# Performance work log

Measured on AMD Instinct MI355X. Metric: run time of the kernel, lower is better.

The kernel has to match this reference:

```python
import jax, jax.numpy as jnp
import numpy as np

B, D, L = 8, 512, 2000          # batch, encoder_out_dim, seq_len
E = 300                          # embedding_dim
N1, N2 = 118, 8929               # hierarchy level sizes


def setup_inputs() -> dict:
    key = jax.random.key(0)
    k = jax.random.split(key, 6)
    H = jax.random.normal(k[0], (B, D, L), dtype=jnp.float32)
    Q1w = jax.random.normal(k[1], (N1, E), dtype=jnp.float32) * 0.05   # cat_embedding_matrix
    Q2w = jax.random.normal(k[2], (N2, E), dtype=jnp.float32) * 0.05   # label_embedding_matrix
    # Q12: xavier_uniform over [N2, N1]
    bound = float(np.sqrt(6.0 / (N1 + N2)))
    Q12w = jax.random.uniform(k[3], (N2, N1), minval=-bound, maxval=bound, dtype=jnp.float32)
    # 1x1 conv mapping: weight [D, E], bias [D] (kernel_size=1 squeezed)
    cbound = float(np.sqrt(1.0 / E))
    Wmap = jax.random.uniform(k[4], (D, E), minval=-cbound, maxval=cbound, dtype=jnp.float32)
    bmap = jax.random.uniform(k[5], (D,), minval=-cbound, maxval=cbound, dtype=jnp.float32)
    return {"H": H, "Q1w": Q1w, "Q2w": Q2w, "Q12w": Q12w, "Wmap": Wmap, "bmap": bmap}


def reference(H, Q1w, Q2w, Q12w, Wmap, bmap):
    # 1x1 conv mapping == affine map over embedding dim: [n, E] @ [E, D] + b
    Q1 = Q1w @ Wmap.T + bmap                      # [N1, D]
    E1 = jnp.einsum('nd,bdl->bnl', Q1, H)         # level-1 scores [B, N1, L]
    A1 = jax.nn.softmax(E1, axis=2)
    C1 = jnp.einsum('bnl,bdl->bnd', A1, H)        # [B, N1, D]
    C1 = jnp.einsum('mn,bnd->bmd', Q12w, C1)      # project to level 2: [B, N2, D]
    Q2 = (Q2w @ Wmap.T + bmap) * C1               # [N2, D] * [B, N2, D]
    E2 = jnp.einsum('bmd,bdl->bml', Q2, H)        # level-2 scores [B, N2, L]
    A2 = jax.nn.softmax(E2, axis=2)
    C2 = jnp.einsum('bml,bdl->bmd', A2, H)        # [B, N2, D]
    return (C2, A2)
```

## Files before the change

### kernel.cpp

```cpp
#include <hip/hip_runtime.h>

typedef short    bf16x8 __attribute__((ext_vector_type(8)));
typedef float    f32x4  __attribute__((ext_vector_type(4)));
typedef unsigned short u16x8 __attribute__((ext_vector_type(8)));

__device__ __forceinline__ unsigned short f2bf(float f) {
    unsigned u = __float_as_uint(f);
    return (unsigned short)((u + 0x7fffu + ((u >> 16) & 1u)) >> 16);
}
__device__ __forceinline__ float bf2f(unsigned short h) {
    return __uint_as_float((unsigned)h << 16);
}

template<bool> struct otype            { using T = float; };
template<>     struct otype<true>      { using T = unsigned short; };

template<int BM,int BN,int TM,int TN,bool BT,bool VA,bool VB,bool OB>
__launch_bounds__(256)
__global__ void gemm_f32(const float* __restrict__ A, int lda, long long sA,
                         const float* __restrict__ B, int ldb, long long sB,
                         void* __restrict__ Cv, int ldc, long long sC,
                         int M, int N, int K,
                         const float* __restrict__ bias,
                         const float* __restrict__ mul, int mulld)
{
    constexpr int BK  = 16;
    constexpr int GSA = BM*4/TM;
    constexpr int GSB = BN*4/TN;
    __shared__ float As[BK][BM+4];
    __shared__ float Bs[BK][BN+4];

    const int bz = blockIdx.z;
    A += (long long)bz * sA;
    B += (long long)bz * sB;
    using OT = typename otype<OB>::T;
    OT* C = (OT*)Cv + (long long)bz * sC;
    const int m0 = blockIdx.y * BM;
    const int n0 = blockIdx.x * BN;
    const int tid = threadIdx.x;
    const int tm = tid >> 4;
    const int tn = tid & 15;

    float acc[TM][TN];
#pragma unroll
    for (int i=0;i<TM;++i)
#pragma unroll
        for (int j=0;j<TN;++j) acc[i][j]=0.f;

    for (int k0=0;k0<K;k0+=BK) {
        if constexpr (VA) {
#pragma unroll
            for (int r=0;r<BM*BK/1024;++r) {
                int v = tid + r*256;
                int m = v >> 2, k4 = (v & 3)*4;
                int gm = m0+m, gk = k0+k4;
                float4 val = make_float4(0.f,0.f,0.f,0.f);
                if (gm < M) {
                    if (gk+3 < K) {
                        val = *reinterpret_cast<const float4*>(A + (long long)gm*lda + gk);
                    } else {
                        float t0 = (gk   < K) ? A[(long long)gm*lda+gk  ] : 0.f;
                        float t1 = (gk+1 < K) ? A[(long long)gm*lda+gk+1] : 0.f;
                        float t2 = (gk+2 < K) ? A[(long long)gm*lda+gk+2] : 0.f;
                        val = make_float4(t0,t1,t2,0.f);
                    }
                }
                As[k4+0][m]=val.x; As[k4+1][m]=val.y; As[k4+2][m]=val.z; As[k4+3][m]=val.w;
            }
        } else {
#pragma unroll
            for (int r=0;r<BM*BK/256;++r) {
                int e = tid + r*256;
                int m = e >> 4, k = e & 15;
                int gm=m0+m, gk=k0+k;
                As[k][m] = (gm<M && gk<K) ? A[(long long)gm*lda+gk] : 0.f;
            }
        }
        if constexpr (!BT) {
            if constexpr (VB) {
#pragma unroll
                for (int r=0;r<BK*BN/1024;++r) {
                    int v = tid + r*256;
                    int k = v / (BN/4), n4 = (v % (BN/4))*4;
                    int gk=k0+k, gn=n0+n4;
                    float4 val = make_float4(0.f,0.f,0.f,0.f);
                    if (gk < K) {
                        if (gn+3 < N) {
                            val = *reinterpret_cast<const float4*>(B + (long long)gk*ldb + gn);
                        } else {
                            float t0=(gn  <N)?B[(long long)gk*ldb+gn  ]:0.f;
                            float t1=(gn+1<N)?B[(long long)gk*ldb+gn+1]:0.f;
                            float t2=(gn+2<N)?B[(long long)gk*ldb+gn+2]:0.f;
                            val = make_float4(t0,t1,t2,0.f);
                        }
                    }
                    Bs[k][n4+0]=val.x; Bs[k][n4+1]=val.y; Bs[k][n4+2]=val.z; Bs[k][n4+3]=val.w;
                }
            } else {
#pragma unroll
                for (int r=0;r<BK*BN/256;++r) {
                    int e = tid + r*256;
                    int k = e / BN, n = e % BN;
                    int gk=k0+k, gn=n0+n;
                    Bs[k][n] = (gk<K && gn<N) ? B[(long long)gk*ldb+gn] : 0.f;
                }
            }
        } else {
            if constexpr (VB) {
#pragma unroll
                for (int r=0;r<BN*BK/1024;++r) {
                    int v = tid + r*256;
                    int n = v >> 2, k4 = (v&3)*4;
                    int gn=n0+n, gk=k0+k4;
                    float4 val = make_float4(0.f,0.f,0.f,0.f);
                    if (gn < N) {
                        if (gk+3 < K) {
                            val = *reinterpret_cast<const float4*>(B + (long long)gn*ldb + gk);
                        } else {
                            float t0=(gk  <K)?B[(long long)gn*ldb+gk  ]:0.f;
                            float t1=(gk+1<K)?B[(long long)gn*ldb+gk+1]:0.f;
                            float t2=(gk+2<K)?B[(long long)gn*ldb+gk+2]:0.f;
                            val=make_float4(t0,t1,t2,0.f);
                        }
                    }
                    Bs[k4+0][n]=val.x; Bs[k4+1][n]=val.y; Bs[k4+2][n]=val.z; Bs[k4+3][n]=val.w;
                }
            } else {
#pragma unroll
                for (int r=0;r<BN*BK/256;++r) {
                    int e = tid + r*256;
                    int n = e >> 4, k = e & 15;
                    int gn=n0+n, gk=k0+k;
                    Bs[k][n] = (gn<N && gk<K) ? B[(long long)gn*ldb+gk] : 0.f;
                }
            }
        }
        __syncthreads();
#pragma unroll
        for (int kk=0;kk<BK;++kk) {
            float a[TM], bb[TN];
#pragma unroll
            for (int g=0;g<TM/4;++g) {
                float4 t = *reinterpret_cast<const float4*>(&As[kk][g*GSA + tm*4]);
                a[4*g+0]=t.x; a[4*g+1]=t.y; a[4*g+2]=t.z; a[4*g+3]=t.w;
            }
#pragma unroll
            for (int g=0;g<TN/4;++g) {
                float4 t = *reinterpret_cast<const float4*>(&Bs[kk][g*GSB + tn*4]);
                bb[4*g+0]=t.x; bb[4*g+1]=t.y; bb[4*g+2]=t.z; bb[4*g+3]=t.w;
            }
#pragma unroll
            for (int i=0;i<TM;++i)
#pragma unroll
                for (int j=0;j<TN;++j)
                    acc[i][j] = fmaf(a[i], bb[j], acc[i][j]);
        }
        __syncthreads();
    }
#pragma unroll
    for (int i=0;i<TM;++i) {
        int row = m0 + (i>>2)*GSA + tm*4 + (i&3);
        if (row < M) {
#pragma unroll
            for (int j=0;j<TN;++j) {
                int col = n0 + (j>>2)*GSB + tn*4 + (j&3);
                if (col < N) {
                    float val = acc[i][j];
                    if (bias) val += bias[col];
                    if (mul)  val *= mul[(long long)row*mulld + col];
                    if constexpr (OB) C[(long long)row*ldc + col] = f2bf(val);
                    else              C[(long long)row*ldc + col] = val;
                }
            }
        }
    }
}

template<unsigned F>
__launch_bounds__(512, 4)
__global__ void gemm_mfma_p(const unsigned short* __restrict__ A, int lda, long long sA,
                            const unsigned short* __restrict__ Bt, int ldb, long long sB,
                            void* __restrict__ Cv, int ldc, long long sC,
                            int M, int Ncols, int NX, int NY, int NT,
                            const float* __restrict__ bias,
                            const float* __restrict__ mul, int ldm,
                            float* __restrict__ partial, long long pstride,
                            const float* __restrict__ hsum,
                            const float* __restrict__ invs,
                            float* __restrict__ a2out,
                            float* __restrict__ dump)
{
    __shared__ unsigned short lds[3][12288];

    const int nwg = gridDim.x;
    const int q = nwg >> 3, r = nwg & 7;
    const int xcd = blockIdx.x & 7, idx = blockIdx.x >> 3;
    const int wg = (xcd < r ? xcd*(q+1) : r*(q+1) + (xcd-r)*q) + idx;
    const int nx = wg % NX;
    const int t1 = wg / NX;
    const int my = t1 % NY;
    const int bz = t1 / NY;

    const int tid  = threadIdx.x;
    const int lane = tid & 63, wid = tid >> 6;
    const int wr = wid >> 2, wc = wid & 3;
    const int fr = lane & 15, fq = lane >> 4;
    const int m0 = my * 128;
    const int n0 = nx * 256;

    A  += (long long)bz * sA;
    Bt += (long long)bz * sB;

    const int srow = tid >> 2;
    const int scz  = (tid & 3) ^ ((srow >> 1) & 3);
    long long arow = m0 + srow; if (arow > M-1) arow = M-1;
    const unsigned short* aSrc  = A  + arow*lda + scz*8;
    const unsigned short* bSrc0 = Bt + (long long)(n0 + srow)*ldb + scz*8;
    const unsigned short* bSrc1 = bSrc0 + 128ll*ldb;

    bool a2ok = false;
    int  par  = 0;
    float invv = 0.f;
    float* a2p = nullptr;
    if constexpr ((F & 64) != 0) {
        par = nx & 1;
        const int rrow = m0 + srow;
        a2ok = rrow < M;
        const long long ridx = (long long)bz*M + (a2ok ? rrow : M-1);
        invv = invs[ridx];
        asm volatile("" : "+v"(invv));
        a2p = a2out + ridx*2000ll;
    }

    int aoff[4], boff[4];
#pragma unroll
    for (int m=0;m<4;++m) {
        const int ra = wr*64 + m*16 + fr;
        aoff[m] = ra*64 + ((fq ^ ((ra>>1)&3))*16);
    }
#pragma unroll
    for (int n=0;n<4;++n) {
        const int rb = wc*64 + n*16 + fr;
        boff[n] = 8192 + rb*64 + ((fq ^ ((rb>>1)&3))*16);
    }

    f32x4 acc[4][4];
#pragma unroll
    for (int i=0;i<4;++i)
#pragma unroll
        for (int j=0;j<4;++j) acc[i][j] = (f32x4)(0.f);

    auto stage = [&](int s, int t) {
        const int koff = t*32;
        char* base = (char*)&lds[s][0];
        __builtin_amdgcn_global_load_lds(
            (const __attribute__((address_space(1))) void*)(aSrc + koff),
            (__attribute__((address_space(3))) void*)(base + tid*16), 16, 0, 0);
        __builtin_amdgcn_global_load_lds(
            (const __attribute__((address_space(1))) void*)(bSrc0 + koff),
            (__attribute__((address_space(3))) void*)(base + 8192 + tid*16), 16, 0, 0);
        __builtin_amdgcn_global_load_lds(
            (const __attribute__((address_space(1))) void*)(bSrc1 + koff),
            (__attribute__((address_space(3))) void*)(base + 16384 + tid*16), 16, 0, 0);
    };

    stage(0, 0);
    stage(1, NT > 1 ? 1 : 0);
    asm volatile("s_waitcnt vmcnt(3)" ::: "memory");
    __builtin_amdgcn_s_barrier();

    int cur = 0, stg = 2;
    for (int kt = 0; kt < NT; ++kt) {
        int tnx = kt + 2; if (tnx > NT-1) tnx = NT-1;
        stage(stg, tnx);
        const char* bp = (const char*)&lds[cur][0];
        bf16x8 a[4], b[4];
#pragma unroll
        for (int m=0;m<4;++m) a[m] = *(const bf16x8*)(bp + aoff[m]);
#pragma unroll
        for (int n=0;n<4;++n) b[n] = *(const bf16x8*)(bp + boff[n]);
        __builtin_amdgcn_s_setprio(1);
#pragma unroll
        for (int m=0;m<4;++m)
#pragma unroll
            for (int n=0;n<4;++n)
                acc[m][n] = __builtin_amdgcn_mfma_f32_16x16x32_bf16(a[m], b[n], acc[m][n], 0, 0, 0);
        __builtin_amdgcn_s_setprio(0);
        if constexpr ((F & 64) != 0) {
            if ((kt & 1) == par) {
                u16x8 av = *(const u16x8*)(bp + (tid << 4));
                const int col0 = kt*32 + scz*8;
                const bool ok = a2ok && (col0 < 2000);
                float* p0 = ok ? (a2p + col0) : (dump + (tid << 3));
                float4 o0, o1;
                o0.x = fmaf(bf2f((unsigned short)av[0]), invv, invv);
                o0.y = fmaf(bf2f((unsigned short)av[1]), invv, invv);
                o0.z = fmaf(bf2f((unsigned short)av[2]), invv, invv);
                o0.w = fmaf(bf2f((unsigned short)av[3]), invv, invv);
                o1.x = fmaf(bf2f((unsigned short)av[4]), invv, invv);
                o1.y = fmaf(bf2f((unsigned short)av[5]), invv, invv);
                o1.z = fmaf(bf2f((unsigned short)av[6]), invv, invv);
                o1.w = fmaf(bf2f((unsigned short)av[7]), invv, invv);
                *(float4*)(p0    ) = o0;
                *(float4*)(p0 + 4) = o1;
            }
        }
        asm volatile("s_waitcnt lgkmcnt(0)" ::: "memory");
        if constexpr ((F & 64) != 0) {
            asm volatile("s_waitcnt vmcnt(5)" ::: "memory");
        } else {
            asm volatile("s_waitcnt vmcnt(3)" ::: "memory");
        }
        __builtin_amdgcn_s_barrier();
        cur = (cur == 2) ? 0 : cur + 1;
        stg = (stg == 2) ? 0 : stg + 1;
    }

    if constexpr ((F & 16) != 0) {
        __shared__ float sp[4][128];
        unsigned short* Cb = (unsigned short*)Cv + (long long)bz * sC;
        float rp[4][4];
#pragma unroll
        for (int m=0;m<4;++m)
#pragma unroll
            for (int j=0;j<4;++j) rp[m][j] = 0.f;
#pragma unroll
        for (int m=0;m<4;++m) {
            const int rb = m0 + wr*64 + m*16 + fq*4;
#pragma unroll
            for (int n=0;n<4;++n) {
                const int col = n0 + wc*64 + n*16 + fr;
#pragma unroll
                for (int j=0;j<4;++j) {
                    float x = __expf(acc[m][n][j]) - 1.0f;
                    rp[m][j] += x;
                    const int row = rb + j;
                    if (row < M) Cb[(long long)row*ldc + col] = f2bf(x);
                }
            }
        }
#pragma unroll
        for (int m=0;m<4;++m)
#pragma unroll
            for (int j=0;j<4;++j) {
                float s = rp[m][j];
                s += __shfl_xor(s, 1); s += __shfl_xor(s, 2);
                s += __shfl_xor(s, 4); s += __shfl_xor(s, 8);
                rp[m][j] = s;
            }
        if (fr == 0) {
#pragma unroll
            for (int m=0;m<4;++m)
#pragma unroll
                for (int j=0;j<4;++j)
                    sp[wc][wr*64 + m*16 + fq*4 + j] = rp[m][j];
        }
        __syncthreads();
        if (tid < 128) {
            const int row = m0 + tid;
            if (row < M) {
                float s = sp[0][tid] + sp[1][tid] + sp[2][tid] + sp[3][tid];
                partial[(long long)nx*pstride + (long long)bz*M + row] = s;
            }
        }
    } else if constexpr ((F & 8) != 0) {
        unsigned short* Ct = (unsigned short*)Cv + (long long)bz * sC;
#pragma unroll
        for (int m=0;m<4;++m) {
            const int rb = m0 + wr*64 + m*16 + fq*4;
#pragma unroll
            for (int n=0;n<4;++n) {
                const int col = n0 + wc*64 + n*16 + fr;
                if (col < Ncols) {
                    float hv = 0.f;
                    if constexpr ((F & 32) != 0) hv = hsum[(long long)bz*Ncols + col];
#pragma unroll
                    for (int j=0;j<4;++j) {
                        const int row = rb + j;
                        float val = 0.f;
                        if (row < M) {
                            val = acc[m][n][j];
                            if constexpr ((F & 32) != 0) val = (val + hv) * invs[(long long)bz*M + row];
                        }
                        Ct[(long long)col*ldc + row] = f2bf(val);
                    }
                }
            }
        }
    } else {
        float*          Cf = (float*)Cv + (long long)bz * sC;
        unsigned short* Cb = (unsigned short*)Cv + (long long)bz * sC;
#pragma unroll
        for (int m=0;m<4;++m) {
            const int rb = m0 + wr*64 + m*16 + fq*4;
#pragma unroll
            for (int n=0;n<4;++n) {
                const int col = n0 + wc*64 + n*16 + fr;
                if (col < Ncols) {
                    float bv = 0.f, hv = 0.f;
                    if constexpr ((F & 1) != 0) bv = bias[col];
                    if constexpr ((F & 32) != 0) hv = hsum[(long long)bz*Ncols + col];
#pragma unroll
                    for (int j=0;j<4;++j) {
                        const int row = rb + j;
                        if (row < M) {
                            float val = acc[m][n][j];
                            if constexpr ((F & 1)   != 0) val += bv;
                            if constexpr ((F & 2)   != 0) val *= mul[(long long)row*ldm + col];
                            if constexpr ((F & 128) != 0) val *= bf2f(((const unsigned short*)mul)[(long long)row*ldm + col]);
                            if constexpr ((F & 32)  != 0) val = (val + hv) * invs[(long long)bz*M + row];
                            if constexpr ((F & 4)   != 0) Cb[(long long)row*ldc + col] = f2bf(val);
                            else                          Cf[(long long)row*ldc + col] = val;
                        }
                    }
                }
            }
        }
    }
}

template<bool AF32>
__launch_bounds__(512, 2)
__global__ void gemm_mfma(const void* __restrict__ Ain, int lda, long long sA,
                          const unsigned short* __restrict__ Bt, int ldb, long long sB,
                          float* __restrict__ C, int ldc, long long sC,
                          int M, int N, int K, int NT)
{
    __shared__ unsigned short As[2][128*32];
    __shared__ unsigned short Bs[2][256*32];

    const int tid  = threadIdx.x;
    const int lane = tid & 63, wid = tid >> 6;
    const int wr = wid >> 2, wc = wid & 3;
    const int fr = lane & 15, fq = lane >> 4;
    const int bz = blockIdx.z;
    const int m0 = blockIdx.y * 128;
    const int n0 = blockIdx.x * 256;

    const unsigned short* Ab = nullptr;
    const float*          Af = nullptr;
    if constexpr (AF32) Af = (const float*)Ain + (long long)bz * sA;
    else                Ab = (const unsigned short*)Ain + (long long)bz * sA;
    Bt += (long long)bz * sB;
    C  += (long long)bz * sC;

    const int srow = tid >> 2;
    const int sc   = tid & 3;
    const int scz  = sc ^ ((srow >> 1) & 3);
    int arow = m0 + srow; if (arow > M-1) arow = M-1;
    const bool am_ok = (m0 + srow) < M;
    const long long brow0 = n0 + srow;
    const long long brow1 = n0 + 128 + srow;
    const int ldsA  = wid << 10;
    const int ldsB0 = wid << 10;
    const int ldsB1 = 8192 + (wid << 10);

    f32x4 acc[4][4];
#pragma unroll
    for (int i=0;i<4;++i)
#pragma unroll
        for (int j=0;j<4;++j) acc[i][j] = (f32x4)(0.f);

    auto stage = [&](int buf, int t) {
        const long long koff = (long long)t * 32;
        __builtin_amdgcn_global_load_lds(
            (const __attribute__((address_space(1))) void*)(Bt + brow0*ldb + koff + scz*8),
            (__attribute__((address_space(3))) void*)((char*)&Bs[buf][0] + ldsB0), 16, 0, 0);
        __builtin_amdgcn_global_load_lds(
            (const __attribute__((address_space(1))) void*)(Bt + brow1*ldb + koff + scz*8),
            (__attribute__((address_space(3))) void*)((char*)&Bs[buf][0] + ldsB1), 16, 0, 0);
        if constexpr (!AF32) {
            __builtin_amdgcn_global_load_lds(
                (const __attribute__((address_space(1))) void*)(Ab + (long long)arow*lda + koff + scz*8),
                (__attribute__((address_space(3))) void*)((char*)&As[buf][0] + ldsA), 16, 0, 0);
        } else {
            const float* src = Af + (long long)arow*lda + koff + scz*8;
            const int kk = t*32 + scz*8;
            float4 z = make_float4(0.f,0.f,0.f,0.f);
            float4 v0 = (am_ok && kk   < K) ? *(const float4*)(src  ) : z;
            float4 v1 = (am_ok && kk+4 < K) ? *(const float4*)(src+4) : z;
            u16x8 o;
            o[0]=f2bf(v0.x); o[1]=f2bf(v0.y); o[2]=f2bf(v0.z); o[3]=f2bf(v0.w);
            o[4]=f2bf(v1.x); o[5]=f2bf(v1.y); o[6]=f2bf(v1.z); o[7]=f2bf(v1.w);
            *(u16x8*)((char*)&As[buf][0] + tid*16) = o;
        }
    };

    stage(0, 0);
    int cur = 0;
    for (int t = 0; t < NT; ++t) {
        __syncthreads();
        if (t + 1 < NT) stage(cur ^ 1, t + 1);
        const unsigned short* as = As[cur];
        const unsigned short* bs = Bs[cur];
        bf16x8 a[4], b[4];
#pragma unroll
        for (int m=0;m<4;++m) {
            const int ra = wr*64 + m*16 + fr;
            a[m] = *(const bf16x8*)(as + ra*32 + (fq ^ ((ra>>1)&3))*8);
        }
#pragma unroll
        for (int n=0;n<4;++n) {
            const int rb = wc*64 + n*16 + fr;
            b[n] = *(const bf16x8*)(bs + rb*32 + (fq ^ ((rb>>1)&3))*8);
        }
        __builtin_amdgcn_s_setprio(1);
#pragma unroll
        for (int m=0;m<4;++m)
#pragma unroll
            for (int n=0;n<4;++n)
                acc[m][n] = __builtin_amdgcn_mfma_f32_16x16x32_bf16(a[m], b[n], acc[m][n], 0, 0, 0);
        __builtin_amdgcn_s_setprio(0);
        cur ^= 1;
    }
#pragma unroll
    for (int m=0;m<4;++m) {
        const int rb = m0 + wr*64 + m*16 + fq*4;
#pragma unroll
        for (int n=0;n<4;++n) {
            const int col = n0 + wc*64 + n*16 + fr;
            if (col < N) {
#pragma unroll
                for (int j=0;j<4;++j) {
                    const int row = rb + j;
                    if (row < M) C[(long long)row*ldc + col] = acc[m][n][j];
                }
            }
        }
    }
}

__global__ __launch_bounds__(256) void mega_prep(const float* __restrict__ H,
                                                 unsigned short* __restrict__ Hb,
                                                 unsigned short* __restrict__ Htb,
                                                 float* __restrict__ hpart,
                                                 const float* __restrict__ Wmap,  unsigned short* __restrict__ Wb,
                                                 const float* __restrict__ Q1w,   unsigned short* __restrict__ Q1wb,
                                                 const float* __restrict__ Q2w,   unsigned short* __restrict__ Q2wb,
                                                 const float* __restrict__ Q12w,  unsigned short* __restrict__ Q12wb)
{
    __shared__ unsigned short T[64][80];
    const int tid = threadIdx.x;
    int id = blockIdx.x;
    if (id < 2048) {
        const int lt = id & 31;
        const int dt = (id >> 5) & 7;
        const int bz = id >> 8;
        const int d0 = dt * 64;
        const int l0 = lt * 64;
        const float* Hsrc = H + ((long long)bz*512 + d0) * 2000;
        const int dl = tid >> 2;
        const int lc = (tid & 3) * 16;
        float4 v[4];
        float s = 0.f;
#pragma unroll
        for (int i=0;i<4;++i) {
            const int gl = l0 + lc + i*4;
            v[i] = make_float4(0.f,0.f,0.f,0.f);
            if (gl < 2000) v[i] = *(const float4*)(Hsrc + (long long)dl*2000 + gl);
            s += (v[i].x + v[i].y) + (v[i].z + v[i].w);
            T[lc+i*4+0][dl] = f2bf(v[i].x);
            T[lc+i*4+1][dl] = f2bf(v[i].y);
            T[lc+i*4+2][dl] = f2bf(v[i].z);
            T[lc+i*4+3][dl] = f2bf(v[i].w);
        }
        {
            unsigned short* hb = Hb + ((long long)bz*512 + d0 + dl)*2048 + l0 + lc;
            u16x8 h0, h1;
            h0[0]=f2bf(v[0].x); h0[1]=f2bf(v[0].y); h0[2]=f2bf(v[0].z); h0[3]=f2bf(v[0].w);
            h0[4]=f2bf(v[1].x); h0[5]=f2bf(v[1].y); h0[6]=f2bf(v[1].z); h0[7]=f2bf(v[1].w);
            h1[0]=f2bf(v[2].x); h1[1]=f2bf(v[2].y); h1[2]=f2bf(v[2].z); h1[3]=f2bf(v[2].w);
            h1[4]=f2bf(v[3].x); h1[5]=f2bf(v[3].y); h1[6]=f2bf(v[3].z); h1[7]=f2bf(v[3].w);
            *(u16x8*)(hb    ) = h0;
            *(u16x8*)(hb + 8) = h1;
        }
        s += __shfl_xor(s, 1);
        s += __shfl_xor(s, 2);
        if ((tid & 3) == 0)
            hpart[(long long)lt*4096 + bz*512 + d0 + dl] = s;
        __syncthreads();
        unsigned short* Hdst = Htb + ((long long)bz*2048 + l0) * 512 + d0;
        const int ll = tid >> 2;
        const int dc = (tid & 3) * 16;
        u16x8 w0 = *(const u16x8*)&T[ll][dc];
        u16x8 w1 = *(const u16x8*)&T[ll][dc+8];
        *(u16x8*)(Hdst + (long long)ll*512 + dc    ) = w0;
        *(u16x8*)(Hdst + (long long)ll*512 + dc + 8) = w1;
        return;
    }
    id -= 2048;
    const float* src; unsigned short* dst; long long tot; int sc, dc;
    if (id < 640)        { src=Wmap;  dst=Wb;    tot=512ll*320;  sc=300; dc=320; }
    else if (id < 788)   { id-=640;   src=Q1w;   dst=Q1wb;  tot=118ll*320;  sc=300; dc=320; }
    else if (id < 11950) { id-=788;   src=Q2w;   dst=Q2wb;  tot=8929ll*320; sc=300; dc=320; }
    else                 { id-=11950; src=Q12w;  dst=Q12wb; tot=8929ll*128; sc=118; dc=128; }
    const long long i = (long long)id*256 + tid;
    if (i < tot) {
        const long long rr = i / dc;
        const int c = (int)(i - rr*dc);
        dst[i] = (c < sc) ? f2bf(src[rr*sc + c]) : (unsigned short)0;
    }
}

__global__ __launch_bounds__(256) void reduce_hsum(const float* __restrict__ hpart,
                                                   float* __restrict__ Hsum)
{
    const int r = blockIdx.x*256 + threadIdx.x;
    float s = 0.f;
#pragma unroll
    for (int i=0;i<32;++i) s += hpart[(long long)i*4096 + r];
    Hsum[r] = s;
}

__global__ __launch_bounds__(256) void invs_k(const float* __restrict__ partial,
                                              long long pstride,
                                              float* __restrict__ invs, int n)
{
    const int r = blockIdx.x*256 + threadIdx.x;
    if (r < n) {
        float s = 0.f;
#pragma unroll
        for (int i=0;i<8;++i) s += partial[i*pstride + r];
        invs[r] = 1.0f / (2000.0f + s);
    }
}

__global__ __launch_bounds__(256) void cvt_pad_bf16(const float* __restrict__ H,
                                                    unsigned short* __restrict__ Hb)
{
    const long long idx = (long long)blockIdx.x * 256 + threadIdx.x;
    const long long row = idx >> 8;
    const int l0 = (int)(idx & 255) * 8;
    u16x8 o = (u16x8)(unsigned short)0;
    if (l0 + 8 <= 2000) {
        const float* s = H + row*2000 + l0;
        float4 v0 = *(const float4*)(s);
        float4 v1 = *(const float4*)(s+4);
        o[0]=f2bf(v0.x); o[1]=f2bf(v0.y); o[2]=f2bf(v0.z); o[3]=f2bf(v0.w);
        o[4]=f2bf(v1.x); o[5]=f2bf(v1.y); o[6]=f2bf(v1.z); o[7]=f2bf(v1.w);
    }
    *(u16x8*)(Hb + row*2048 + l0) = o;
}

__global__ __launch_bounds__(256) void cvt_transpose_bf16(const float* __restrict__ H,
                                                          unsigned short* __restrict__ Ht)
{
    __shared__ unsigned short T[64][80];
    const int bz = blockIdx.z;
    const int d0 = blockIdx.y * 64;
    const int l0 = blockIdx.x * 64;
    const float* Hsrc = H + ((long long)bz*512 + d0) * 2000;
    unsigned short* Hdst = Ht + ((long long)bz*2048 + l0) * 512 + d0;
    const int tid = threadIdx.x;
    const int dl = tid >> 2;
    const int lc = (tid & 3) * 16;
#pragma unroll
    for (int i=0;i<4;++i) {
        const int l = lc + i*4;
        const int gl = l0 + l;
        float4 v = make_float4(0.f,0.f,0.f,0.f);
        if (gl < 2000) v = *(const float4*)(Hsrc + (long long)dl*2000 + gl);
        T[l+0][dl] = f2bf(v.x);
        T[l+1][dl] = f2bf(v.y);
        T[l+2][dl] = f2bf(v.z);
        T[l+3][dl] = f2bf(v.w);
    }
    __syncthreads();
    const int ll = tid >> 2;
    const int dc = (tid & 3) * 16;
    u16x8 w0 = *(const u16x8*)&T[ll][dc];
    u16x8 w1 = *(const u16x8*)&T[ll][dc+8];
    *(u16x8*)(Hdst + (long long)ll*512 + dc    ) = w0;
    *(u16x8*)(Hdst + (long long)ll*512 + dc + 8) = w1;
}

__global__ __launch_bounds__(256) void softmax_rows(float* __restrict__ X, int L,
                                                    unsigned short* __restrict__ Xb, int Lb)
{
    const long long row = blockIdx.x;
    float* x = X + row * (long long)L;
    const int tid = threadIdx.x;
    const int nv = L >> 2;
    const bool h0 = tid < nv;
    const bool h1 = tid + 256 < nv;
    float4 t0 = make_float4(0.f,0.f,0.f,0.f);
    float4 t1 = make_float4(0.f,0.f,0.f,0.f);
    float mx = -3.402823e38f;
    if (h0) { t0 = *reinterpret_cast<const float4*>(x + 4*tid);
              mx = fmaxf(fmaxf(t0.x,t0.y), fmaxf(t0.z,t0.w)); }
    if (h1) { t1 = *reinterpret_cast<const float4*>(x + 4*(tid+256));
              mx = fmaxf(mx, fmaxf(fmaxf(t1.x,t1.y), fmaxf(t1.z,t1.w))); }
    __shared__ float sred[4];
#pragma unroll
    for (int o=32;o;o>>=1) mx = fmaxf(mx, __shfl_xor(mx, o));
    if ((tid & 63)==0) sred[tid>>6] = mx;
    __syncthreads();
    mx = fmaxf(fmaxf(sred[0],sred[1]), fmaxf(sred[2],sred[3]));
    __syncthreads();
    float s = 0.f;
    if (h0) {
        t0.x=__expf(t0.x-mx); t0.y=__expf(t0.y-mx); t0.z=__expf(t0.z-mx); t0.w=__expf(t0.w-mx);
        s += (t0.x+t0.y)+(t0.z+t0.w);
    }
    if (h1) {
        t1.x=__expf(t1.x-mx); t1.y=__expf(t1.y-mx); t1.z=__expf(t1.z-mx); t1.w=__expf(t1.w-mx);
        s += (t1.x+t1.y)+(t1.z+t1.w);
    }
#pragma unroll
    for (int o=32;o;o>>=1) s += __shfl_xor(s, o);
    if ((tid & 63)==0) sred[tid>>6] = s;
    __syncthreads();
    s = (sred[0]+sred[1])+(sred[2]+sred[3]);
    const float inv = 1.0f / s;
    if (h0) { t0.x*=inv; t0.y*=inv; t0.z*=inv; t0.w*=inv;
              *reinterpret_cast<float4*>(x + 4*tid) = t0; }
    if (h1) { t1.x*=inv; t1.y*=inv; t1.z*=inv; t1.w*=inv;
              *reinterpret_cast<float4*>(x + 4*(tid+256)) = t1; }
    if (Xb) {
        unsigned short* xb = Xb + row * (long long)Lb;
        if (h0) {
            ushort4 o; o.x=f2bf(t0.x); o.y=f2bf(t0.y); o.z=f2bf(t0.z); o.w=f2bf(t0.w);
            *reinterpret_cast<ushort4*>(xb + 4*tid) = o;
        }
        if (h1) {
            ushort4 o; o.x=f2bf(t1.x); o.y=f2bf(t1.y); o.z=f2bf(t1.z); o.w=f2bf(t1.w);
            *reinterpret_cast<ushort4*>(xb + 4*(tid+256)) = o;
        }
        if (tid < (Lb - L)/4) {
            ushort4 z; z.x=z.y=z.z=z.w=0;
            *reinterpret_cast<ushort4*>(xb + L + 4*tid) = z;
        }
    }
}

extern "C" void kernel_launch(void* const* d_in, const int* in_sizes, int n_in,
                              void* d_out, int out_size, void* d_ws, size_t ws_size,
                              hipStream_t stream)
{
    const float* H    = (const float*)d_in[0];
    const float* Q1w  = (const float*)d_in[1];
    const float* Q2w  = (const float*)d_in[2];
    const float* Q12w = (const float*)d_in[3];
    const float* Wmap = (const float*)d_in[4];
    const float* bmap = (const float*)d_in[5];

    constexpr long long B=8, D=512, L=2000, N1=118, N2=8929;
    constexpr long long C2E = B*N2*D;
    float* out = (float*)d_out;
    float* C2  = out;
    float* A2  = out + C2E;

    dim3 blk(256);

    size_t off = 0;
    auto alloc = [&](size_t n)->size_t { off = (off + 255) & ~(size_t)255; size_t o = off; off += n; return o; };
    const size_t oHb    = alloc(8ll*512*2048*2);
    const size_t oHtb   = alloc(8ll*2048*512*2);
    const size_t oWb    = alloc(512ll*320*2);
    const size_t oQ1wb  = alloc(118ll*320*2);
    const size_t oQ2wb  = alloc(8929ll*320*2);
    const size_t oQ12wb = alloc(8929ll*128*2);
    const size_t oQ1b   = alloc(118ll*512*2);
    const size_t oEmbb  = alloc(8929ll*512*2);
    const size_t oE1x   = alloc(8ll*128*2048*2);
    const size_t oC1tb  = alloc(8ll*512*128*2);
    const size_t oQ2b   = alloc(8ll*8929*512*2);
    const size_t oA2b   = alloc(8ll*8929*2048*2);
    const size_t oPart  = alloc(8ll*8*8929*4);
    const size_t oPart1 = alloc(8ll*944*4);
    const size_t oInvs  = alloc(8ll*8929*4);
    const size_t oInvs1 = alloc(944ll*4);
    const size_t oHsum  = alloc(8ll*512*4);
    const size_t oHpart = alloc(32ll*4096*4);
    const size_t FULL_NEED = off;

    char* ws = (char*)d_ws;

    if (ws_size >= FULL_NEED) {
        unsigned short* Hb    = (unsigned short*)(ws + oHb);
        unsigned short* Htb   = (unsigned short*)(ws + oHtb);
        unsigned short* Wb    = (unsigned short*)(ws + oWb);
        unsigned short* Q1wb  = (unsigned short*)(ws + oQ1wb);
        unsigned short* Q2wb  = (unsigned short*)(ws + oQ2wb);
        unsigned short* Q12wb = (unsigned short*)(ws + oQ12wb);
        unsigned short* Q1b   = (unsigned short*)(ws + oQ1b);
        unsigned short* Embb  = (unsigned short*)(ws + oEmbb);
        unsigned short* E1x   = (unsigned short*)(ws + oE1x);
        unsigned short* C1tb  = (unsigned short*)(ws + oC1tb);
        unsigned short* Q2b   = (unsigned short*)(ws + oQ2b);
        unsigned short* A2b   = (unsigned short*)(ws + oA2b);
        float*          part  = (float*)(ws + oPart);
        float*          part1 = (float*)(ws + oPart1);
        float*          invs  = (float*)(ws + oInvs);
        float*          invs1 = (float*)(ws + oInvs1);
        float*          Hsum  = (float*)(ws + oHsum);
        float*          hpart = (float*)(ws + oHpart);

        mega_prep<<<dim3(18464), blk, 0, stream>>>(H, Hb, Htb, hpart,
                                                   Wmap, Wb, Q1w, Q1wb, Q2w, Q2wb, Q12w, Q12wb);
        reduce_hsum<<<dim3(16), blk, 0, stream>>>(hpart, Hsum);

        gemm_mfma_p<5><<<dim3(2), dim3(512), 0, stream>>>(
            Q1wb, 320, 0, Wb, 320, 0, Q1b, 512, 0, 118, 512, 2, 1, 10,
            bmap, nullptr, 0, nullptr, 0, nullptr, nullptr, nullptr, nullptr);
        gemm_mfma_p<5><<<dim3(140), dim3(512), 0, stream>>>(
            Q2wb, 320, 0, Wb, 320, 0, Embb, 512, 0, 8929, 512, 2, 70, 10,
            bmap, nullptr, 0, nullptr, 0, nullptr, nullptr, nullptr, nullptr);
        gemm_mfma_p<16><<<dim3(64), dim3(512), 0, stream>>>(
            Q1b, 512, 0, Htb, 512, 2048*512, E1x, 2048, 128*2048, 118, 2048, 8, 1, 16,
            nullptr, nullptr, 0, part1, 944, nullptr, nullptr, nullptr, nullptr);
        invs_k<<<dim3(4), blk, 0, stream>>>(part1, 944, invs1, 944);
        gemm_mfma_p<40><<<dim3(16), dim3(512), 0, stream>>>(
            E1x, 2048, 128*2048, Hb, 2048, 512*2048, C1tb, 128, 512*128, 118, 512, 2, 1, 64,
            nullptr, nullptr, 0, nullptr, 0, Hsum, invs1, nullptr, nullptr);
        gemm_mfma_p<132><<<dim3(1120), dim3(512), 0, stream>>>(
            Q12wb, 128, 0, C1tb, 128, 512*128, Q2b, 512, N2*D, 8929, 512, 2, 70, 4,
            nullptr, (const float*)Embb, 512, nullptr, 0, nullptr, nullptr, nullptr, nullptr);
        gemm_mfma_p<16><<<dim3(4480), dim3(512), 0, stream>>>(
            Q2b, 512, N2*D, Htb, 512, 2048*512, A2b, 2048, N2*2048, 8929, 2048, 8, 70, 16,
            nullptr, nullptr, 0, part, 8ll*8929, nullptr, nullptr, nullptr, nullptr);
        invs_k<<<dim3(280), blk, 0, stream>>>(part, 8ll*8929, invs, (int)(B*N2));
        gemm_mfma_p<96><<<dim3(1120), dim3(512), 0, stream>>>(
            A2b, 2048, N2*2048, Hb, 2048, 512*2048, C2, 512, N2*D, 8929, 512, 2, 70, 64,
            nullptr, nullptr, 0, nullptr, 0, Hsum, invs, A2, part);
        return;
    }

    float* Q1  = A2;
    float* emb = Q1  + N1*D;
    float* E1  = emb + N2*D;
    float* C1  = E1  + B*N1*L;

    gemm_f32<64,64,4,4,true,true,true,false><<<dim3(8,2,1), blk, 0, stream>>>(
        Q1w, 300, 0, Wmap, 300, 0, Q1, 512, 0, (int)N1, (int)D, 300, bmap, nullptr, 0);
    gemm_f32<64,64,4,4,true,true,true,false><<<dim3(8,140,1), blk, 0, stream>>>(
        Q2w, 300, 0, Wmap, 300, 0, emb, 512, 0, (int)N2, (int)D, 300, bmap, nullptr, 0);
    gemm_f32<64,64,4,4,false,true,true,false><<<dim3(32,2,8), blk, 0, stream>>>(
        Q1, 512, 0, H, 2000, D*L, E1, 2000, N1*L, (int)N1, (int)L, (int)D, nullptr, nullptr, 0);
    softmax_rows<<<dim3((unsigned)(B*N1)), blk, 0, stream>>>(E1, (int)L, nullptr, 0);
    gemm_f32<64,64,4,4,true,true,true,false><<<dim3(8,2,8), blk, 0, stream>>>(
        E1, 2000, N1*L, H, 2000, D*L, C1, 512, N1*D, (int)N1, (int)D, (int)L, nullptr, nullptr, 0);

    constexpr long long HBE = 8ll*512*2048;
    if (ws_size >= (size_t)(2*HBE*sizeof(unsigned short))) {
        unsigned short* Hb  = (unsigned short*)d_ws;
        unsigned short* Htb = Hb + HBE;
        cvt_pad_bf16<<<dim3(4096), blk, 0, stream>>>(H, Hb);
        cvt_transpose_bf16<<<dim3(32,8,8), blk, 0, stream>>>(H, Htb);
        unsigned short* Q2b = (unsigned short*)C2;
        gemm_f32<64,64,4,4,false,false,true,true><<<dim3(8,140,8), blk, 0, stream>>>(
            Q12w, 118, 0, C1, 512, N1*D, Q2b, 512, N2*D, (int)N2, (int)D, (int)N1, nullptr, emb, 512);
        gemm_mfma_p<0><<<dim3(4480), dim3(512), 0, stream>>>(
            Q2b, 512, N2*D, Htb, 512, 2048*512, A2, 2000, N2*L, (int)N2, (int)L, 8, 70, 16,
            nullptr, nullptr, 0, nullptr, 0, nullptr, nullptr, nullptr, nullptr);
        softmax_rows<<<dim3((unsigned)(B*N2)), blk, 0, stream>>>(A2, (int)L, nullptr, 0);
        gemm_mfma<true><<<dim3(2,70,8), dim3(512), 0, stream>>>(
            A2, 2000, N2*L, Hb, 2048, 512*2048, C2, 512, N2*D,
            (int)N2, (int)D, 2000, 63);
    } else {
        float* Q2 = C2;
        gemm_f32<64,64,4,4,false,false,true,false><<<dim3(8,140,8), blk, 0, stream>>>(
            Q12w, 118, 0, C1, 512, N1*D, Q2, 512, N2*D, (int)N2, (int)D, (int)N1, nullptr, emb, 512);
        gemm_f32<128,128,8,8,false,true,true,false><<<dim3(16,70,8), blk, 0, stream>>>(
            Q2, 512, N2*D, H, 2000, D*L, A2, 2000, N2*L, (int)N2, (int)L, (int)D, nullptr, nullptr, 0);
        softmax_rows<<<dim3((unsigned)(B*N2)), blk, 0, stream>>>(A2, (int)L, nullptr, 0);
        gemm_f32<128,128,8,8,true,true,true,false><<<dim3(4,70,8), blk, 0, stream>>>(
            A2, 2000, N2*L, H, 2000, D*L, C2, 512, N2*D, (int)N2, (int)D, (int)L, nullptr, nullptr, 0);
    }
}
```

Before: 822.9 us.

## Stage bf16 GEMM epilogues through swizzled LDS and move A2 writes to column-zero blocks

The exp epilogue and the bf16-output epilogue now write results into swizzled shared memory and then store full 16-byte rows to global memory. Row sums are computed from the staged bf16 values instead of through a shuffle and shared-memory reduction. A2 output writing is handed only to nx==0 blocks, instead of being split across block parity, so other blocks wait with a lighter vmcnt. The conversion kernel also gets per-source branches with constant divisors. The intent is to cut uncoalesced 2-byte global stores and the 64-bit index math, at the cost of an extra barrier and LDS round trip, plus load imbalance on the A2-writing blocks.

```diff
diff --git a/kernel.cpp b/kernel.cpp
--- a/kernel.cpp
+++ b/kernel.cpp
@@ -218,18 +218,19 @@
     const unsigned short* bSrc0 = Bt + (long long)(n0 + srow)*ldb + scz*8;
     const unsigned short* bSrc1 = bSrc0 + 128ll*ldb;
 
-    bool a2ok = false;
-    int  par  = 0;
+    bool wrblk = false, a2ok = false;
     float invv = 0.f;
     float* a2p = nullptr;
     if constexpr ((F & 64) != 0) {
-        par = nx & 1;
-        const int rrow = m0 + srow;
-        a2ok = rrow < M;
-        const long long ridx = (long long)bz*M + (a2ok ? rrow : M-1);
-        invv = invs[ridx];
-        asm volatile("" : "+v"(invv));
-        a2p = a2out + ridx*2000ll;
+        wrblk = (nx == 0);
+        if (wrblk) {
+            const int rrow = m0 + srow;
+            a2ok = rrow < M;
+            const long long ridx = (long long)bz*M + (a2ok ? rrow : M-1);
+            invv = invs[ridx];
+            asm volatile("" : "+v"(invv));
+            a2p = a2out + ridx*2000ll;
+        }
     }
 
     int aoff[4], boff[4];
@@ -287,7 +288,7 @@
                 acc[m][n] = __builtin_amdgcn_mfma_f32_16x16x32_bf16(a[m], b[n], acc[m][n], 0, 0, 0);
         __builtin_amdgcn_s_setprio(0);
         if constexpr ((F & 64) != 0) {
-            if ((kt & 1) == par) {
+            if (wrblk) {
                 u16x8 av = *(const u16x8*)(bp + (tid << 4));
                 const int col0 = kt*32 + scz*8;
                 const bool ok = a2ok && (col0 < 2000);
@@ -307,7 +308,8 @@
         }
         asm volatile("s_waitcnt lgkmcnt(0)" ::: "memory");
         if constexpr ((F & 64) != 0) {
-            asm volatile("s_waitcnt vmcnt(5)" ::: "memory");
+            if (wrblk) asm volatile("s_waitcnt vmcnt(5)" ::: "memory");
+            else       asm volatile("s_waitcnt vmcnt(3)" ::: "memory");
         } else {
             asm volatile("s_waitcnt vmcnt(3)" ::: "memory");
         }
@@ -317,51 +319,46 @@
     }
 
     if constexpr ((F & 16) != 0) {
-        __shared__ float sp[4][128];
+        asm volatile("s_waitcnt vmcnt(0)" ::: "memory");
+        __builtin_amdgcn_s_barrier();
+        unsigned short* ep = (unsigned short*)&lds[0][0];
         unsigned short* Cb = (unsigned short*)Cv + (long long)bz * sC;
-        float rp[4][4];
-#pragma unroll
-        for (int m=0;m<4;++m)
-#pragma unroll
-            for (int j=0;j<4;++j) rp[m][j] = 0.f;
 #pragma unroll
         for (int m=0;m<4;++m) {
-            const int rb = m0 + wr*64 + m*16 + fq*4;
+            const int rl = wr*64 + m*16 + fq*4;
 #pragma unroll
             for (int n=0;n<4;++n) {
-                const int col = n0 + wc*64 + n*16 + fr;
+                const int cl = wc*64 + n*16 + fr;
+                const int cb = cl*2;
 #pragma unroll
                 for (int j=0;j<4;++j) {
+                    const int row = rl + j;
                     float x = __expf(acc[m][n][j]) - 1.0f;
-                    rp[m][j] += x;
-                    const int row = rb + j;
-                    if (row < M) Cb[(long long)row*ldc + col] = f2bf(x);
-                }
-            }
-        }
-#pragma unroll
-        for (int m=0;m<4;++m)
-#pragma unroll
-            for (int j=0;j<4;++j) {
-                float s = rp[m][j];
-                s += __shfl_xor(s, 1); s += __shfl_xor(s, 2);
-                s += __shfl_xor(s, 4); s += __shfl_xor(s, 8);
-                rp[m][j] = s;
-            }
-        if (fr == 0) {
-#pragma unroll
-            for (int m=0;m<4;++m)
-#pragma unroll
-                for (int j=0;j<4;++j)
-                    sp[wc][wr*64 + m*16 + fq*4 + j] = rp[m][j];
+                    const int ch = (cb>>5) ^ ((row>>2)&3);
+                    *(unsigned short*)((char*)ep + row*512 + (ch<<5) + (cb&31)) = f2bf(x);
+                }
+            }
         }
         __syncthreads();
-        if (tid < 128) {
-            const int row = m0 + tid;
-            if (row < M) {
-                float s = sp[0][tid] + sp[1][tid] + sp[2][tid] + sp[3][tid];
-                partial[(long long)nx*pstride + (long long)bz*M + row] = s;
-            }
+        const int rq = tid >> 3;
+        const int cq = tid & 7;
+#pragma unroll
+        for (int half=0; half<2; ++half) {
+            const int row = rq + half*64;
+            const int grow = m0 + row;
+            float s = 0.f;
+#pragma unroll
+            for (int win=0; win<4; ++win) {
+                const int cb = cq*16 + win*128;
+                const int ch = (cb>>5) ^ ((row>>2)&3);
+                u16x8 v = *(const u16x8*)((const char*)ep + row*512 + (ch<<5) + (cb&31));
+#pragma unroll
+                for (int i=0;i<8;++i) s += bf2f((unsigned short)v[i]);
+                if (grow < M) *(u16x8*)(Cb + (long long)grow*ldc + n0 + (cb>>1)) = v;
+            }
+            s += __shfl_xor(s, 1); s += __shfl_xor(s, 2); s += __shfl_xor(s, 4);
+            if (cq == 0 && grow < M)
+                partial[(long long)nx*pstride + (long long)bz*M + grow] = s;
         }
     } else if constexpr ((F & 8) != 0) {
         unsigned short* Ct = (unsigned short*)Cv + (long long)bz * sC;
@@ -387,9 +384,57 @@
                 }
             }
         }
+    } else if constexpr ((F & 4) != 0) {
+        asm volatile("s_waitcnt vmcnt(0)" ::: "memory");
+        __builtin_amdgcn_s_barrier();
+        unsigned short* ep = (unsigned short*)&lds[0][0];
+        unsigned short* Cb = (unsigned short*)Cv + (long long)bz * sC;
+#pragma unroll
+        for (int m=0;m<4;++m) {
+            const int rl = wr*64 + m*16 + fq*4;
+#pragma unroll
+            for (int n=0;n<4;++n) {
+                const int cl = wc*64 + n*16 + fr;
+                const int gcol = n0 + cl;
+                const int cb = cl*2;
+                float bv = 0.f;
+                if constexpr ((F & 1) != 0) bv = bias[gcol];
+#pragma unroll
+                for (int j=0;j<4;++j) {
+                    const int row = rl + j;
+                    float val = acc[m][n][j];
+                    if constexpr ((F & 1) != 0) val += bv;
+                    if constexpr ((F & 128) != 0) {
+                        int mr = m0 + row; if (mr > M-1) mr = M-1;
+                        val *= bf2f(((const unsigned short*)mul)[(long long)mr*ldm + gcol]);
+                    }
+                    if constexpr ((F & 2) != 0) {
+                        int mr = m0 + row; if (mr > M-1) mr = M-1;
+                        val *= mul[(long long)mr*ldm + gcol];
+                    }
+                    const int ch = (cb>>5) ^ ((row>>2)&3);
+                    *(unsigned short*)((char*)ep + row*512 + (ch<<5) + (cb&31)) = f2bf(val);
+                }
+            }
+        }
+        __syncthreads();
+        const int rq = tid >> 3;
+        const int cq = tid & 7;
+#pragma unroll
+        for (int half=0; half<2; ++half) {
+            const int row = rq + half*64;
+            const int grow = m0 + row;
+#pragma unroll
+            for (int win=0; win<4; ++win) {
+                const int cb = cq*16 + win*128;
+                const int ch = (cb>>5) ^ ((row>>2)&3);
+                u16x8 v = *(const u16x8*)((const char*)ep + row*512 + (ch<<5) + (cb&31));
+                const int gc = n0 + (cb>>1);
+                if (grow < M && gc < Ncols) *(u16x8*)(Cb + (long long)grow*ldc + gc) = v;
+            }
+        }
     } else {
-        float*          Cf = (float*)Cv + (long long)bz * sC;
-        unsigned short* Cb = (unsigned short*)Cv + (long long)bz * sC;
+        float* Cf = (float*)Cv + (long long)bz * sC;
 #pragma unroll
         for (int m=0;m<4;++m) {
             const int rb = m0 + wr*64 + m*16 + fq*4;
@@ -409,8 +454,7 @@
                             if constexpr ((F & 2)   != 0) val *= mul[(long long)row*ldm + col];
                             if constexpr ((F & 128) != 0) val *= bf2f(((const unsigned short*)mul)[(long long)row*ldm + col]);
                             if constexpr ((F & 32)  != 0) val = (val + hv) * invs[(long long)bz*M + row];
-                            if constexpr ((F & 4)   != 0) Cb[(long long)row*ldc + col] = f2bf(val);
-                            else                          Cf[(long long)row*ldc + col] = val;
+                            Cf[(long long)row*ldc + col] = val;
                         }
                     }
                 }
@@ -589,16 +633,30 @@
         return;
     }
     id -= 2048;
-    const float* src; unsigned short* dst; long long tot; int sc, dc;
-    if (id < 640)        { src=Wmap;  dst=Wb;    tot=512ll*320;  sc=300; dc=320; }
-    else if (id < 788)   { id-=640;   src=Q1w;   dst=Q1wb;  tot=118ll*320;  sc=300; dc=320; }
-    else if (id < 11950) { id-=788;   src=Q2w;   dst=Q2wb;  tot=8929ll*320; sc=300; dc=320; }
-    else                 { id-=11950; src=Q12w;  dst=Q12wb; tot=8929ll*128; sc=118; dc=128; }
-    const long long i = (long long)id*256 + tid;
-    if (i < tot) {
-        const long long rr = i / dc;
-        const int c = (int)(i - rr*dc);
-        dst[i] = (c < sc) ? f2bf(src[rr*sc + c]) : (unsigned short)0;
+    if (id < 640) {
+        const int i = id*256 + tid;
+        if (i < 512*320) {
+            const int r2 = i/320, c = i - r2*320;
+            Wb[i] = (c < 300) ? f2bf(Wmap[r2*300 + c]) : (unsigned short)0;
+        }
+    } else if (id < 788) {
+        const int i = (id-640)*256 + tid;
+        if (i < 118*320) {
+            const int r2 = i/320, c = i - r2*320;
+            Q1wb[i] = (c < 300) ? f2bf(Q1w[r2*300 + c]) : (unsigned short)0;
+        }
+    } else if (id < 11950) {
+        const int i = (id-788)*256 + tid;
+        if (i < 8929*320) {
+            const int r2 = i/320, c = i - r2*320;
+            Q2wb[i] = (c < 300) ? f2bf(Q2w[r2*300 + c]) : (unsigned short)0;
+        }
+    } else {
+        const int i = (id-11950)*256 + tid;
+        if (i < 8929*128) {
+            const int r2 = i >> 7, c = i & 127;
+            Q12wb[i] = (c < 118) ? f2bf(Q12w[r2*118 + c]) : (unsigned short)0;
+        }
     }
 }
 
```

Result: faster. 732.8 us (-10.9%).
